# Kernel optimization log

Hardware: AMD Instinct MI355X
Metric: run time of the kernel (lower is better)

The kernel has to match this reference:

```python
import jax, jax.numpy as jnp
import numpy as np

N_NODES = 100000
N_EDGES = 800000
IN_CH = 128
HID = 128
OUT_CH = 64


def setup_inputs() -> dict:
    key = jax.random.key(0)
    ks = jax.random.split(key, 8)
    x = jax.random.normal(ks[0], (N_NODES, IN_CH), dtype=jnp.float32)
    edge_index = jax.random.randint(ks[1], (2, N_EDGES), 0, N_NODES, dtype=jnp.int64)
    # GCNConv weights (Glorot) and zero biases
    def glorot(k, fan_in, fan_out):
        s = jnp.sqrt(6.0 / (fan_in + fan_out))
        return jax.random.uniform(k, (fan_in, fan_out), jnp.float32, -s, s)
    return {
        "x": x,
        "edge_index": edge_index,
        "W1": glorot(ks[2], IN_CH, HID), "b1": jnp.zeros((HID,), jnp.float32),
        "W2": glorot(ks[3], HID, HID),   "b2": jnp.zeros((HID,), jnp.float32),
        "W3": glorot(ks[4], HID, OUT_CH), "b3": jnp.zeros((OUT_CH,), jnp.float32),
    }


def _gcn_conv(h, W, b, src, dst, norm, self_norm, n_nodes):
    """PyG GCNConv: out = D^-1/2 (A+I) D^-1/2 (h W) + b.
    Self-loop contribution added densely (self_norm = dinv^2) to avoid
    appending N extra edges."""
    h = h @ W  # [N, F_out]
    msg = h[src] * norm[:, None]  # [E, F_out] gathered + normalized messages
    agg = jax.ops.segment_sum(msg, dst, num_segments=n_nodes)
    return agg + h * self_norm[:, None] + b


def reference(x, edge_index, W1, b1, W2, b2, W3, b3):
    n_nodes = x.shape[0]
    src = edge_index[0]
    dst = edge_index[1]
    # degrees with self-loops (edge weights = 1)
    deg = jax.ops.segment_sum(jnp.ones_like(src, dtype=x.dtype), dst,
                              num_segments=n_nodes) + 1.0
    dinv = jax.lax.rsqrt(deg)
    norm = dinv[src] * dinv[dst]   # per-edge symmetric normalization
    self_norm = dinv * dinv        # normalization of the i->i self loop

    h = jax.nn.relu(_gcn_conv(x, W1, b1, src, dst, norm, self_norm, n_nodes))
    # dropout is identity in eval mode (training=False)
    h = jax.nn.relu(_gcn_conv(h, W2, b2, src, dst, norm, self_norm, n_nodes))
    out = _gcn_conv(h, W3, b3, src, dst, norm, self_norm, n_nodes)
    return out
```

## Files before the change

kernel.cpp:

```cpp
#include <hip/hip_runtime.h>


#define IN_CH 128

typedef __attribute__((ext_vector_type(8))) short bf16x8;
typedef __attribute__((ext_vector_type(4))) float f32x4;

__device__ inline unsigned short f2bf_rne(float f) {
    unsigned u = __float_as_uint(f);
    unsigned r = (u + 0x7FFFu + ((u >> 16) & 1u)) >> 16;
    return (unsigned short)r;
}
__device__ inline float bf2f(unsigned short h) {
    return __uint_as_float(((unsigned)h) << 16);
}
__device__ inline float bf2f_lo(unsigned m) {
    return __uint_as_float(m << 16);
}
__device__ inline float bf2f_hi(unsigned m) {
    return __uint_as_float(m & 0xffff0000u);
}

__global__ __launch_bounds__(256) void cnt_k(const int* __restrict__ dst,
                                             int* __restrict__ cnt, int E) {
    int e = blockIdx.x * 256 + threadIdx.x;
    if (e < E) atomicAdd(&cnt[dst[e]], 1);
}

__global__ __launch_bounds__(256) void scan1_k(const int* __restrict__ cnt,
                                               int* __restrict__ bsum,
                                               float* __restrict__ dinv, int N) {
    __shared__ int s[256];
    int tid = threadIdx.x;
    int i = blockIdx.x * 256 + tid;
    int vr = (i < N) ? cnt[i] : 0;
    if (i < N) dinv[i] = rsqrtf((float)vr + 1.0f);
    s[tid] = (i < N) ? ((vr + 3) & ~3) : 0;
    __syncthreads();
    for (int off = 128; off > 0; off >>= 1) {
        if (tid < off) s[tid] += s[tid + off];
        __syncthreads();
    }
    if (tid == 0) bsum[blockIdx.x] = s[0];
}

__global__ __launch_bounds__(512) void scan2_k(int* __restrict__ bsum, int nb) {
    __shared__ int s[512];
    __shared__ int carry_s;
    int tid = threadIdx.x;
    if (tid == 0) carry_s = 0;
    __syncthreads();
    for (int base = 0; base < nb; base += 512) {
        int c = carry_s;
        int i = base + tid;
        int v = (i < nb) ? bsum[i] : 0;
        s[tid] = v;
        __syncthreads();
        for (int off = 1; off < 512; off <<= 1) {
            int t = (tid >= off) ? s[tid - off] : 0;
            __syncthreads();
            s[tid] += t;
            __syncthreads();
        }
        if (i < nb) bsum[i] = s[tid] - v + c;
        __syncthreads();
        if (tid == 0) carry_s = c + s[511];
        __syncthreads();
    }
}

__global__ __launch_bounds__(256) void scan3_k(const int* __restrict__ cnt,
                                               const int* __restrict__ bsum,
                                               int* __restrict__ rowstart,
                                               int* __restrict__ cur, int N) {
    __shared__ int s[256];
    int tid = threadIdx.x;
    int i = blockIdx.x * 256 + tid;
    int v = (i < N) ? ((cnt[i] + 3) & ~3) : 0;
    s[tid] = v;
    __syncthreads();
    for (int off = 1; off < 256; off <<= 1) {
        int t = (tid >= off) ? s[tid - off] : 0;
        __syncthreads();
        s[tid] += t;
        __syncthreads();
    }
    if (i < N) {
        int st = s[tid] - v + bsum[blockIdx.x];
        rowstart[i] = st;
        cur[i] = st;
        if (i == N - 1) rowstart[N] = st + v;
    }
}

__device__ inline void convw_one(const float* W, unsigned short* hi, int FOUT, int id) {
    int n = id >> 7, k = id & 127;
    hi[id] = f2bf_rne(W[k * FOUT + n]);
}

__global__ __launch_bounds__(256) void fill_conv_k(
    const int* __restrict__ src, const int* __restrict__ dst,
    const float* __restrict__ dinv, int* __restrict__ cur,
    int2* __restrict__ pairs, int E, int fillBlocks,
    const float* __restrict__ W1, const float* __restrict__ W2,
    const float* __restrict__ W3,
    unsigned short* __restrict__ W1h, unsigned short* __restrict__ W2h,
    unsigned short* __restrict__ W3h) {
    if ((int)blockIdx.x < fillBlocks) {
        int e = blockIdx.x * 256 + threadIdx.x;
        if (e < E) {
            int s = src[e], d = dst[e];
            float nrm = dinv[s] * dinv[d];
            int pos = atomicAdd(&cur[d], 1);
            pairs[pos] = make_int2(s * 256, __float_as_int(nrm));
        }
    } else {
        int id = (blockIdx.x - fillBlocks) * 256 + threadIdx.x;
        if (id < 16384) convw_one(W1, W1h, 128, id);
        else if (id < 32768) convw_one(W2, W2h, 128, id - 16384);
        else if (id < 40960) convw_one(W3, W3h, 64, id - 32768);
    }
}

__device__ inline bf16x8 cvt8(const float* __restrict__ p) {
    float4 v0 = *(const float4*)p;
    float4 v1 = *(const float4*)(p + 4);
    bf16x8 h;
    h[0] = (short)f2bf_rne(v0.x); h[1] = (short)f2bf_rne(v0.y);
    h[2] = (short)f2bf_rne(v0.z); h[3] = (short)f2bf_rne(v0.w);
    h[4] = (short)f2bf_rne(v1.x); h[5] = (short)f2bf_rne(v1.y);
    h[6] = (short)f2bf_rne(v1.z); h[7] = (short)f2bf_rne(v1.w);
    return h;
}

template <int FOUT, bool AF32>
__global__ __launch_bounds__(256) void mfma_gemm(const float* __restrict__ Af,
                                                 const unsigned short* __restrict__ Ahi,
                                                 const unsigned short* __restrict__ Bhi,
                                                 unsigned short* __restrict__ Thi,
                                                 int N) {
    constexpr int NCT = FOUT / 16;
    constexpr int BSTRIDE = 136;
    constexpr int CSTRIDE = FOUT + 8;
    constexpr int BU = FOUT * BSTRIDE;
    constexpr int CU = 64 * CSTRIDE;
    constexpr int SMEMU = (BU > CU) ? BU : CU;
    __shared__ unsigned short smem[SMEMU];

    const int tid = threadIdx.x;
    const int wv = tid >> 6, lane = tid & 63;
    const int quad = lane >> 4, l16 = lane & 15;
    const int row0 = blockIdx.x * 64 + wv * 16;

#pragma unroll
    for (int it = 0; it < FOUT / 16; ++it) {
        int i = it * 256 + tid;
        int r = i >> 4, c = (i & 15) * 8;
        *(bf16x8*)(&smem[r * BSTRIDE + c]) = *(const bf16x8*)(Bhi + (size_t)r * 128 + c);
    }
    __syncthreads();

    f32x4 acc[NCT];
#pragma unroll
    for (int ct = 0; ct < NCT; ++ct)
        acc[ct] = (f32x4){0.f, 0.f, 0.f, 0.f};

    const int ra = AF32 ? min(row0 + l16, N - 1) : (row0 + l16);

#pragma unroll
    for (int ks = 0; ks < 4; ++ks) {
        const int ko = ks * 32 + quad * 8;
        bf16x8 ah;
        if (AF32) {
            ah = cvt8(Af + (size_t)ra * 128 + ko);
        } else {
            ah = *(const bf16x8*)(Ahi + (size_t)ra * 128 + ko);
        }
#pragma unroll
        for (int ct = 0; ct < NCT; ++ct) {
            bf16x8 bh = *(const bf16x8*)(&smem[(ct * 16 + l16) * BSTRIDE + ko]);
            acc[ct] = __builtin_amdgcn_mfma_f32_16x16x32_bf16(ah, bh, acc[ct], 0, 0, 0);
        }
    }

    __syncthreads();
    const int lrow = wv * 16 + quad * 4;
#pragma unroll
    for (int ct = 0; ct < NCT; ++ct) {
        const int col = ct * 16 + l16;
#pragma unroll
        for (int r = 0; r < 4; ++r)
            smem[(lrow + r) * CSTRIDE + col] = f2bf_rne(acc[ct][r]);
    }
    __syncthreads();
    constexpr int CH = FOUT / 8;
#pragma unroll
    for (int i = 0; i < 64 * CH / 256; ++i) {
        int ci = i * 256 + tid;
        int r = ci / CH, c = (ci % CH) * 8;
        int grow = blockIdx.x * 64 + r;
        if (grow < N)
            *(uint4*)(Thi + (size_t)grow * FOUT + c) = *(const uint4*)&smem[r * CSTRIDE + c];
    }
}

template <int FOUT, bool SPLIT>
__global__ __launch_bounds__(256) void gather_k(const int* __restrict__ rowstart,
                                                const int2* __restrict__ pairs,
                                                const float* __restrict__ dinv,
                                                const unsigned short* __restrict__ Thi,
                                                const float* __restrict__ bias,
                                                float* __restrict__ out,
                                                unsigned short* __restrict__ outHi,
                                                int N) {
    const int wave = threadIdx.x >> 6;
    const int lane = threadIdx.x & 63;
    const int row = blockIdx.x * 4 + wave;
    if (row >= N) return;

    const int start = rowstart[row];
    const int end = rowstart[row + 1];
    const float dr = dinv[row];
    const char* tbase = (const char*)Thi;

    if (FOUT == 128) {
        const int laneB = lane * 4;
        unsigned sh = *(const unsigned*)(tbase + (size_t)row * 256 + laneB);
        float2 bb = *(const float2*)(bias + lane * 2);
        float ax = bb.x + bf2f_lo(sh) * dr * dr;
        float ay = bb.y + bf2f_hi(sh) * dr * dr;

        for (int j = start; j < end; j += 4) {
            int4 p01 = *(const int4*)(pairs + j);
            int4 p23 = *(const int4*)(pairs + j + 2);
            unsigned m0 = *(const unsigned*)(tbase + (unsigned)p01.x + laneB);
            unsigned m1 = *(const unsigned*)(tbase + (unsigned)p01.z + laneB);
            unsigned m2 = *(const unsigned*)(tbase + (unsigned)p23.x + laneB);
            unsigned m3 = *(const unsigned*)(tbase + (unsigned)p23.z + laneB);
            float n0 = __int_as_float(p01.y), n1 = __int_as_float(p01.w);
            float n2 = __int_as_float(p23.y), n3 = __int_as_float(p23.w);
            ax += n0 * bf2f_lo(m0); ay += n0 * bf2f_hi(m0);
            ax += n1 * bf2f_lo(m1); ay += n1 * bf2f_hi(m1);
            ax += n2 * bf2f_lo(m2); ay += n2 * bf2f_hi(m2);
            ax += n3 * bf2f_lo(m3); ay += n3 * bf2f_hi(m3);
        }

        if (SPLIT) {
            float vx = fmaxf(ax, 0.f), vy = fmaxf(ay, 0.f);
            ushort2 h;
            h.x = f2bf_rne(vx);
            h.y = f2bf_rne(vy);
            *(ushort2*)(outHi + (size_t)row * 128 + lane * 2) = h;
        } else {
            float2 o; o.x = ax; o.y = ay;
            *(float2*)(out + (size_t)row * 128 + lane * 2) = o;
        }
    } else {
        const int laneB = lane * 2;
        float acc = bias[lane] +
                    bf2f(*(const unsigned short*)(tbase + (size_t)row * 128 + laneB)) * dr * dr;

        for (int j = start; j < end; j += 4) {
            int4 p01 = *(const int4*)(pairs + j);
            int4 p23 = *(const int4*)(pairs + j + 2);
            float m0 = bf2f(*(const unsigned short*)(tbase + ((unsigned)p01.x >> 1) + laneB));
            float m1 = bf2f(*(const unsigned short*)(tbase + ((unsigned)p01.z >> 1) + laneB));
            float m2 = bf2f(*(const unsigned short*)(tbase + ((unsigned)p23.x >> 1) + laneB));
            float m3 = bf2f(*(const unsigned short*)(tbase + ((unsigned)p23.z >> 1) + laneB));
            acc += __int_as_float(p01.y) * m0 + __int_as_float(p01.w) * m1 +
                   __int_as_float(p23.y) * m2 + __int_as_float(p23.w) * m3;
        }
        out[(size_t)row * FOUT + lane] = acc;
    }
}

extern "C" void kernel_launch(void* const* d_in, const int* in_sizes, int n_in,
                              void* d_out, int out_size, void* d_ws, size_t ws_size,
                              hipStream_t stream) {
    const float* x  = (const float*)d_in[0];
    const int* eidx = (const int*)d_in[1];
    const float* W1 = (const float*)d_in[2];
    const float* b1 = (const float*)d_in[3];
    const float* W2 = (const float*)d_in[4];
    const float* b2 = (const float*)d_in[5];
    const float* W3 = (const float*)d_in[6];
    const float* b3 = (const float*)d_in[7];
    float* out = (float*)d_out;

    const int N = in_sizes[0] / IN_CH;
    const int E = in_sizes[1] / 2;
    const int* src = eidx;
    const int* dst = eidx + E;
    const int Npad = ((N + 127) / 128) * 128;
    const int nb = (N + 255) / 256;
    const int Emax = E + 3 * N;

    auto align = [](size_t v) { return (v + 255) / 256 * 256; };
    char* p = (char*)d_ws;
    int* cnt = (int*)p;            p += align((size_t)N * 4);
    int* rowstart = (int*)p;       p += align((size_t)(N + 1) * 4);
    int* cur = (int*)p;            p += align((size_t)N * 4);
    int* bsum = (int*)p;           p += align((size_t)nb * 4);
    float* dinv = (float*)p;       p += align((size_t)N * 4);
    int2* pairs = (int2*)p;        p += align((size_t)Emax * 8);
    unsigned short* Ahi = (unsigned short*)p;  p += align((size_t)Npad * 128 * 2);
    unsigned short* Thi = (unsigned short*)p;  p += align((size_t)Npad * 128 * 2);
    unsigned short* W1h = (unsigned short*)p;  p += align(128 * 128 * 2);
    unsigned short* W2h = (unsigned short*)p;  p += align(128 * 128 * 2);
    unsigned short* W3h = (unsigned short*)p;

    hipMemsetAsync(cnt, 0, (size_t)N * 4, stream);
    hipMemsetAsync(pairs, 0, (size_t)Emax * 8, stream);
    cnt_k<<<(E + 255) / 256, 256, 0, stream>>>(dst, cnt, E);
    scan1_k<<<nb, 256, 0, stream>>>(cnt, bsum, dinv, N);
    scan2_k<<<1, 512, 0, stream>>>(bsum, nb);
    scan3_k<<<nb, 256, 0, stream>>>(cnt, bsum, rowstart, cur, N);
    const int fillBlocks = (E + 255) / 256;
    fill_conv_k<<<fillBlocks + 160, 256, 0, stream>>>(src, dst, dinv, cur, pairs,
                                                      E, fillBlocks, W1, W2, W3,
                                                      W1h, W2h, W3h);

    const int gemm_blocks = (N + 63) / 64;
    const int gather_blocks = (N + 3) / 4;

    mfma_gemm<128, true><<<gemm_blocks, 256, 0, stream>>>(x, nullptr, W1h, Thi, N);
    gather_k<128, true><<<gather_blocks, 256, 0, stream>>>(rowstart, pairs, dinv, Thi,
                                                           b1, nullptr, Ahi, N);
    mfma_gemm<128, false><<<gemm_blocks, 256, 0, stream>>>(nullptr, Ahi, W2h, Thi, N);
    gather_k<128, true><<<gather_blocks, 256, 0, stream>>>(rowstart, pairs, dinv, Thi,
                                                           b2, nullptr, Ahi, N);
    mfma_gemm<64, false><<<gemm_blocks, 256, 0, stream>>>(nullptr, Ahi, W3h, Thi, N);
    gather_k<64, false><<<gather_blocks, 256, 0, stream>>>(rowstart, pairs, dinv, Thi,
                                                           b3, out, nullptr, N);
}
```

Before: 342.4 us.

## Compress CSR edge entries to 32 bits and split 128-wide gathers into column slices

Each edge pair shrinks from an 8-byte int2 to one 32-bit word: a 17-bit source index plus a 15-bit bf16 normalization. The self-loop is folded into each row's edge list as an explicit entry with weight dinv^2, and row padding moves from a multiple of 4 to a multiple of 8. The zero-fill of padding slots happens inside scan3, so the large memset goes away. The 128-wide gathers now run as 8 column-slice blocks per row group, each wave handling 8 edges in parallel followed by a shuffle reduction; this raises parallelism but reads each row's edge list 8 times. Precision risks include bf16 truncation of the normalization to 15 bits (sign dropped) and node indices limited to 17 bits.

```diff
diff --git a/kernel.cpp b/kernel.cpp
--- a/kernel.cpp
+++ b/kernel.cpp
@@ -35,7 +35,7 @@
     int i = blockIdx.x * 256 + tid;
     int vr = (i < N) ? cnt[i] : 0;
     if (i < N) dinv[i] = rsqrtf((float)vr + 1.0f);
-    s[tid] = (i < N) ? ((vr + 3) & ~3) : 0;
+    s[tid] = (i < N) ? ((vr + 8) & ~7) : 0;
     __syncthreads();
     for (int off = 128; off > 0; off >>= 1) {
         if (tid < off) s[tid] += s[tid + off];
@@ -71,12 +71,15 @@
 
 __global__ __launch_bounds__(256) void scan3_k(const int* __restrict__ cnt,
                                                const int* __restrict__ bsum,
+                                               const float* __restrict__ dinv,
                                                int* __restrict__ rowstart,
-                                               int* __restrict__ cur, int N) {
+                                               int* __restrict__ cur,
+                                               unsigned* __restrict__ cpairs, int N) {
     __shared__ int s[256];
     int tid = threadIdx.x;
     int i = blockIdx.x * 256 + tid;
-    int v = (i < N) ? ((cnt[i] + 3) & ~3) : 0;
+    int cr = (i < N) ? cnt[i] : 0;
+    int v = (i < N) ? ((cr + 8) & ~7) : 0;
     s[tid] = v;
     __syncthreads();
     for (int off = 1; off < 256; off <<= 1) {
@@ -88,8 +91,11 @@
     if (i < N) {
         int st = s[tid] - v + bsum[blockIdx.x];
         rowstart[i] = st;
-        cur[i] = st;
         if (i == N - 1) rowstart[N] = st + v;
+        float dn = dinv[i];
+        cpairs[st] = ((unsigned)i << 15) | (f2bf_rne(dn * dn) & 0x7FFFu);
+        cur[i] = st + 1;
+        for (int k = st + 1 + cr; k < st + v; ++k) cpairs[k] = 0u;
     }
 }
 
@@ -101,7 +107,7 @@
 __global__ __launch_bounds__(256) void fill_conv_k(
     const int* __restrict__ src, const int* __restrict__ dst,
     const float* __restrict__ dinv, int* __restrict__ cur,
-    int2* __restrict__ pairs, int E, int fillBlocks,
+    unsigned* __restrict__ cpairs, int E, int fillBlocks,
     const float* __restrict__ W1, const float* __restrict__ W2,
     const float* __restrict__ W3,
     unsigned short* __restrict__ W1h, unsigned short* __restrict__ W2h,
@@ -112,7 +118,7 @@
             int s = src[e], d = dst[e];
             float nrm = dinv[s] * dinv[d];
             int pos = atomicAdd(&cur[d], 1);
-            pairs[pos] = make_int2(s * 256, __float_as_int(nrm));
+            cpairs[pos] = ((unsigned)s << 15) | (f2bf_rne(nrm) & 0x7FFFu);
         }
     } else {
         int id = (blockIdx.x - fillBlocks) * 256 + threadIdx.x;
@@ -204,74 +210,78 @@
     }
 }
 
-template <int FOUT, bool SPLIT>
-__global__ __launch_bounds__(256) void gather_k(const int* __restrict__ rowstart,
-                                                const int2* __restrict__ pairs,
-                                                const float* __restrict__ dinv,
-                                                const unsigned short* __restrict__ Thi,
-                                                const float* __restrict__ bias,
-                                                float* __restrict__ out,
-                                                unsigned short* __restrict__ outHi,
-                                                int N) {
+template <bool SPLIT>
+__global__ __launch_bounds__(256) void gatherS_k(const int* __restrict__ rowstart,
+                                                 const unsigned* __restrict__ cpairs,
+                                                 const unsigned short* __restrict__ Thi,
+                                                 const float* __restrict__ bias,
+                                                 float* __restrict__ out,
+                                                 unsigned short* __restrict__ outHi,
+                                                 int N) {
+    const int wave = threadIdx.x >> 6;
+    const int lane = threadIdx.x & 63;
+    const int s = blockIdx.x & 7;
+    const int row = (blockIdx.x >> 3) * 4 + wave;
+    if (row >= N) return;
+    const int e = lane >> 3, d = lane & 7;
+    const int start = rowstart[row], end = rowstart[row + 1];
+    const char* tbase = (const char*)Thi;
+    const int colB = s * 32 + d * 4;
+
+    float ax = 0.f, ay = 0.f;
+    for (int j = start; j < end; j += 8) {
+        unsigned p = cpairs[j + e];
+        float n = bf2f((unsigned short)(p & 0x7FFFu));
+        unsigned m = *(const unsigned*)(tbase + ((size_t)(p >> 15) << 8) + colB);
+        ax += n * bf2f_lo(m);
+        ay += n * bf2f_hi(m);
+    }
+    ax += __shfl_xor(ax, 8); ax += __shfl_xor(ax, 16); ax += __shfl_xor(ax, 32);
+    ay += __shfl_xor(ay, 8); ay += __shfl_xor(ay, 16); ay += __shfl_xor(ay, 32);
+
+    if (e == 0) {
+        float2 bb = *(const float2*)(bias + s * 16 + d * 2);
+        ax += bb.x;
+        ay += bb.y;
+        if (SPLIT) {
+            float vx = fmaxf(ax, 0.f), vy = fmaxf(ay, 0.f);
+            unsigned hw = (unsigned)f2bf_rne(vx) | ((unsigned)f2bf_rne(vy) << 16);
+            *(unsigned*)((char*)outHi + (size_t)row * 256 + colB) = hw;
+        } else {
+            float2 o; o.x = ax; o.y = ay;
+            *(float2*)(out + (size_t)row * 128 + s * 16 + d * 2) = o;
+        }
+    }
+}
+
+__global__ __launch_bounds__(256) void gather64_k(const int* __restrict__ rowstart,
+                                                  const unsigned* __restrict__ cpairs,
+                                                  const unsigned short* __restrict__ Thi,
+                                                  const float* __restrict__ bias,
+                                                  float* __restrict__ out, int N) {
     const int wave = threadIdx.x >> 6;
     const int lane = threadIdx.x & 63;
     const int row = blockIdx.x * 4 + wave;
     if (row >= N) return;
-
-    const int start = rowstart[row];
-    const int end = rowstart[row + 1];
-    const float dr = dinv[row];
+    const int start = rowstart[row], end = rowstart[row + 1];
     const char* tbase = (const char*)Thi;
-
-    if (FOUT == 128) {
-        const int laneB = lane * 4;
-        unsigned sh = *(const unsigned*)(tbase + (size_t)row * 256 + laneB);
-        float2 bb = *(const float2*)(bias + lane * 2);
-        float ax = bb.x + bf2f_lo(sh) * dr * dr;
-        float ay = bb.y + bf2f_hi(sh) * dr * dr;
-
-        for (int j = start; j < end; j += 4) {
-            int4 p01 = *(const int4*)(pairs + j);
-            int4 p23 = *(const int4*)(pairs + j + 2);
-            unsigned m0 = *(const unsigned*)(tbase + (unsigned)p01.x + laneB);
-            unsigned m1 = *(const unsigned*)(tbase + (unsigned)p01.z + laneB);
-            unsigned m2 = *(const unsigned*)(tbase + (unsigned)p23.x + laneB);
-            unsigned m3 = *(const unsigned*)(tbase + (unsigned)p23.z + laneB);
-            float n0 = __int_as_float(p01.y), n1 = __int_as_float(p01.w);
-            float n2 = __int_as_float(p23.y), n3 = __int_as_float(p23.w);
-            ax += n0 * bf2f_lo(m0); ay += n0 * bf2f_hi(m0);
-            ax += n1 * bf2f_lo(m1); ay += n1 * bf2f_hi(m1);
-            ax += n2 * bf2f_lo(m2); ay += n2 * bf2f_hi(m2);
-            ax += n3 * bf2f_lo(m3); ay += n3 * bf2f_hi(m3);
-        }
-
-        if (SPLIT) {
-            float vx = fmaxf(ax, 0.f), vy = fmaxf(ay, 0.f);
-            ushort2 h;
-            h.x = f2bf_rne(vx);
-            h.y = f2bf_rne(vy);
-            *(ushort2*)(outHi + (size_t)row * 128 + lane * 2) = h;
-        } else {
-            float2 o; o.x = ax; o.y = ay;
-            *(float2*)(out + (size_t)row * 128 + lane * 2) = o;
-        }
-    } else {
-        const int laneB = lane * 2;
-        float acc = bias[lane] +
-                    bf2f(*(const unsigned short*)(tbase + (size_t)row * 128 + laneB)) * dr * dr;
-
-        for (int j = start; j < end; j += 4) {
-            int4 p01 = *(const int4*)(pairs + j);
-            int4 p23 = *(const int4*)(pairs + j + 2);
-            float m0 = bf2f(*(const unsigned short*)(tbase + ((unsigned)p01.x >> 1) + laneB));
-            float m1 = bf2f(*(const unsigned short*)(tbase + ((unsigned)p01.z >> 1) + laneB));
-            float m2 = bf2f(*(const unsigned short*)(tbase + ((unsigned)p23.x >> 1) + laneB));
-            float m3 = bf2f(*(const unsigned short*)(tbase + ((unsigned)p23.z >> 1) + laneB));
-            acc += __int_as_float(p01.y) * m0 + __int_as_float(p01.w) * m1 +
-                   __int_as_float(p23.y) * m2 + __int_as_float(p23.w) * m3;
-        }
-        out[(size_t)row * FOUT + lane] = acc;
-    }
+    const int laneB = lane * 2;
+    float acc = bias[lane];
+
+    for (int j = start; j < end; j += 8) {
+        uint4 pa = *(const uint4*)(cpairs + j);
+        uint4 pb = *(const uint4*)(cpairs + j + 4);
+        unsigned pp[8] = {pa.x, pa.y, pa.z, pa.w, pb.x, pb.y, pb.z, pb.w};
+        float mv[8], nv[8];
+#pragma unroll
+        for (int k = 0; k < 8; ++k) {
+            nv[k] = bf2f((unsigned short)(pp[k] & 0x7FFFu));
+            mv[k] = bf2f(*(const unsigned short*)(tbase + ((size_t)(pp[k] >> 15) << 7) + laneB));
+        }
+#pragma unroll
+        for (int k = 0; k < 8; ++k) acc += nv[k] * mv[k];
+    }
+    out[(size_t)row * 64 + lane] = acc;
 }
 
 extern "C" void kernel_launch(void* const* d_in, const int* in_sizes, int n_in,
@@ -293,7 +303,7 @@
     const int* dst = eidx + E;
     const int Npad = ((N + 127) / 128) * 128;
     const int nb = (N + 255) / 256;
-    const int Emax = E + 3 * N;
+    const size_t Emax = (size_t)E + 8 * (size_t)N;
 
     auto align = [](size_t v) { return (v + 255) / 256 * 256; };
     char* p = (char*)d_ws;
@@ -302,7 +312,7 @@
     int* cur = (int*)p;            p += align((size_t)N * 4);
     int* bsum = (int*)p;           p += align((size_t)nb * 4);
     float* dinv = (float*)p;       p += align((size_t)N * 4);
-    int2* pairs = (int2*)p;        p += align((size_t)Emax * 8);
+    unsigned* cpairs = (unsigned*)p;  p += align(Emax * 4);
     unsigned short* Ahi = (unsigned short*)p;  p += align((size_t)Npad * 128 * 2);
     unsigned short* Thi = (unsigned short*)p;  p += align((size_t)Npad * 128 * 2);
     unsigned short* W1h = (unsigned short*)p;  p += align(128 * 128 * 2);
@@ -310,26 +320,25 @@
     unsigned short* W3h = (unsigned short*)p;
 
     hipMemsetAsync(cnt, 0, (size_t)N * 4, stream);
-    hipMemsetAsync(pairs, 0, (size_t)Emax * 8, stream);
     cnt_k<<<(E + 255) / 256, 256, 0, stream>>>(dst, cnt, E);
     scan1_k<<<nb, 256, 0, stream>>>(cnt, bsum, dinv, N);
     scan2_k<<<1, 512, 0, stream>>>(bsum, nb);
-    scan3_k<<<nb, 256, 0, stream>>>(cnt, bsum, rowstart, cur, N);
+    scan3_k<<<nb, 256, 0, stream>>>(cnt, bsum, dinv, rowstart, cur, cpairs, N);
     const int fillBlocks = (E + 255) / 256;
-    fill_conv_k<<<fillBlocks + 160, 256, 0, stream>>>(src, dst, dinv, cur, pairs,
+    fill_conv_k<<<fillBlocks + 160, 256, 0, stream>>>(src, dst, dinv, cur, cpairs,
                                                       E, fillBlocks, W1, W2, W3,
                                                       W1h, W2h, W3h);
 
     const int gemm_blocks = (N + 63) / 64;
-    const int gather_blocks = (N + 3) / 4;
+    const int gS_blocks = ((N + 3) / 4) * 8;
+    const int g64_blocks = (N + 3) / 4;
 
     mfma_gemm<128, true><<<gemm_blocks, 256, 0, stream>>>(x, nullptr, W1h, Thi, N);
-    gather_k<128, true><<<gather_blocks, 256, 0, stream>>>(rowstart, pairs, dinv, Thi,
-                                                           b1, nullptr, Ahi, N);
+    gatherS_k<true><<<gS_blocks, 256, 0, stream>>>(rowstart, cpairs, Thi, b1,
+                                                   nullptr, Ahi, N);
     mfma_gemm<128, false><<<gemm_blocks, 256, 0, stream>>>(nullptr, Ahi, W2h, Thi, N);
-    gather_k<128, true><<<gather_blocks, 256, 0, stream>>>(rowstart, pairs, dinv, Thi,
-                                                           b2, nullptr, Ahi, N);
+    gatherS_k<true><<<gS_blocks, 256, 0, stream>>>(rowstart, cpairs, Thi, b2,
+                                                   nullptr, Ahi, N);
     mfma_gemm<64, false><<<gemm_blocks, 256, 0, stream>>>(nullptr, Ahi, W3h, Thi, N);
-    gather_k<64, false><<<gather_blocks, 256, 0, stream>>>(rowstart, pairs, dinv, Thi,
-                                                           b3, out, nullptr, N);
-}
+    gather64_k<<<g64_blocks, 256, 0, stream>>>(rowstart, cpairs, Thi, b3, out, N);
+}
```

Result: slower. 699.4 us (+104.3%).
